# Kernel tuning notes

Hardware: AMD Instinct MI355X
Metric: run time of the kernel (lower is better)

## Reference

```python
import jax, jax.numpy as jnp
import numpy as np

ERR = 1e-6
STIFF_THR = 1e-10
EPS = 1e-12


def _normalize(x, axis=-1):
    n = jnp.linalg.norm(x, axis=axis, keepdims=True)
    return x / jnp.maximum(n, EPS)


def compute_edges(verts):
    # [B, V, 3] -> [B, V-1, 3]
    return verts[:, 1:] - verts[:, :-1]


def compute_kb(edges, restEdgeL):
    # kb[:, i] = 2 e_{i-1} x e_i / (|e_{i-1}||e_i| + e_{i-1}.e_i), kb[:, 0] = 0
    num = 2.0 * jnp.cross(edges[:, :-1], edges[:, 1:])
    den = restEdgeL[:, :-1] * restEdgeL[:, 1:] + jnp.sum(edges[:, :-1] * edges[:, 1:], axis=-1)
    kb = jnp.zeros_like(edges)
    return kb.at[:, 1:].set(num / den[..., None])


def extract_sin_cos(magnitude):
    const = 4.0
    s = jnp.sqrt(magnitude / (magnitude + const))
    c = jnp.sqrt(const / (magnitude + const))
    return s, c


def compute_m_u0(e0, init_direct):
    n0 = jnp.cross(e0, init_direct)
    return _normalize(jnp.cross(n0, e0))


def compute_bishop_frame(u0, edges, restEdgeL):
    # u0 [B,3], edges [B,E,3], restEdgeL [B,E]
    kb = compute_kb(edges, restEdgeL)                 # [B,E,3]
    mag = jnp.sum(kb * kb, axis=-1)                   # [B,E]
    sinP, cosP = extract_sin_cos(mag)
    axis = _normalize(kb)
    qw = cosP                                         # [B,E] quaternion scalar part (half angle)
    qv = sinP[..., None] * axis                       # [B,E,3] quaternion vector part
    v0 = _normalize(jnp.cross(edges[:, 0], u0))

    def step(carry, xs):
        u_p, v_p = carry
        w, xyz, e_i, c = xs                           # [B], [B,3], [B,3], [B]
        t = 2.0 * jnp.cross(xyz, u_p)
        ru = u_p + w[:, None] * t + jnp.cross(xyz, t)  # quaternion rotation of u_{i-1}
        rv = _normalize(jnp.cross(e_i, ru))
        cond = ((1.0 - c) <= ERR)[:, None]
        u_i = jnp.where(cond, u_p, ru)
        v_i = jnp.where(cond, v_p, rv)
        return (u_i, v_i), (u_i, v_i)

    xs = (jnp.swapaxes(qw[:, 1:], 0, 1), jnp.swapaxes(qv[:, 1:], 0, 1),
          jnp.swapaxes(edges[:, 1:], 0, 1), jnp.swapaxes(cosP[:, 1:], 0, 1))
    _, (us, vs) = jax.lax.scan(step, (u0, v0), xs)
    u = jnp.concatenate([u0[:, None], jnp.swapaxes(us, 0, 1)], axis=1)  # [B,E,3]
    v = jnp.concatenate([v0[:, None], jnp.swapaxes(vs, 0, 1)], axis=1)
    return u, v, kb


def compute_w(kb, m1, m2):
    # material-frame curvature: (kb.m2, -kb.m1) -> [.., 2]
    return jnp.stack([jnp.sum(kb * m2, axis=-1), -jnp.sum(kb * m1, axis=-1)], axis=-1)


def compute_material_frame(theta, m1, m2):
    cosQ = jnp.cos(theta)[..., None]
    sinQ = jnp.sin(theta)[..., None]
    m1n = cosQ * m1 + sinQ * m2
    # faithful to torch code: m2 update uses the already-updated m1
    m2n = -sinQ * m1n + cosQ * m2
    return m1n, m2n


def reference(current_vert, init_direct, restEdgeL, restRegionL, m_restWprev,
              m_restWnext, theta_full, bend_stiffness, twist_stiffness):
    edges = compute_edges(current_vert)
    u0 = compute_m_u0(edges[:, 0], init_direct)
    m1, m2, kb = compute_bishop_frame(u0, edges, restEdgeL)
    mat_m1, mat_m2 = compute_material_frame(theta_full, m1, m2)

    # Model_Energy on the (solved) theta_full
    restRegionL_unsq = restRegionL[:, 1:, None]
    oW = compute_w(kb[:, 1:], mat_m1[:, 1:], mat_m2[:, 1:])   # [B,E-1,2]
    dp = oW - m_restWprev[:, 1:]
    dn = oW - m_restWnext[:, 1:]
    bs_last = jnp.maximum(bend_stiffness[:, -1:][..., None], STIFF_THR)   # [1,1,1]
    bs_next = jnp.maximum(bend_stiffness[:, 1:][..., None], STIFF_THR)    # [1,E-1,1]
    energy = jnp.sum(0.5 * (bs_last * dp * dp + bs_next * dn * dn) / restRegionL_unsq, axis=(1, 2))
    m = theta_full[:, 1:] - theta_full[:, :-1]
    energy = energy + jnp.sum(0.5 * jnp.maximum(twist_stiffness[:, 1:], STIFF_THR) * m * m / restRegionL[:, 1:], axis=1)
    return mat_m1, mat_m2, kb, energy[:, None]


def setup_inputs() -> dict:
    key = jax.random.key(0)
    B, V = 32768, 128
    E = V - 1
    ks = jax.random.split(key, 8)
    # near-straight rod along x with small perturbations (keeps kb denominators positive)
    base = jnp.zeros((B, V, 3)).at[:, :, 0].set(jnp.arange(V, dtype=jnp.float32))
    current_vert = base + 0.05 * jax.random.normal(ks[0], (B, V, 3), dtype=jnp.float32)
    init_direct = jax.random.normal(ks[1], (B, 3), dtype=jnp.float32)
    edges = current_vert[:, 1:] - current_vert[:, :-1]
    restEdgeL = jnp.linalg.norm(edges, axis=-1)                       # [B,E]
    restRegionL = jnp.concatenate(
        [restEdgeL[:, :1], 0.5 * (restEdgeL[:, :-1] + restEdgeL[:, 1:])], axis=1)
    m_restWprev = 0.01 * jax.random.normal(ks[2], (B, E, 2), dtype=jnp.float32)
    m_restWnext = 0.01 * jax.random.normal(ks[3], (B, E, 2), dtype=jnp.float32)
    theta_full = 0.1 * jax.random.normal(ks[4], (B, E), dtype=jnp.float32)
    bend_stiffness = 5e-5 * jnp.ones((1, E), dtype=jnp.float32)
    twist_stiffness = 1e-5 * jnp.ones((1, E), dtype=jnp.float32)
    return {"current_vert": current_vert, "init_direct": init_direct,
            "restEdgeL": restEdgeL, "restRegionL": restRegionL,
            "m_restWprev": m_restWprev, "m_restWnext": m_restWnext,
            "theta_full": theta_full, "bend_stiffness": bend_stiffness,
            "twist_stiffness": twist_stiffness}
```

## Files before the change

kernel.cpp:

```cpp
#include <hip/hip_runtime.h>

#define ERRV 1e-6f
#define EPSV 1e-12f
#define THRV 1e-10f
#define MAXV 128

struct F3 { float x, y, z; };

__device__ __forceinline__ F3 mk3(float x, float y, float z){ F3 r; r.x=x; r.y=y; r.z=z; return r; }
__device__ __forceinline__ F3 cross3(F3 a, F3 b){
  return mk3(a.y*b.z - a.z*b.y, a.z*b.x - a.x*b.z, a.x*b.y - a.y*b.x);
}
__device__ __forceinline__ float dot3(F3 a, F3 b){ return a.x*b.x + a.y*b.y + a.z*b.z; }
__device__ __forceinline__ F3 norm3f(F3 a){
  float r = __builtin_amdgcn_rsqf(fmaxf(dot3(a,a), 1e-24f));
  return mk3(a.x*r, a.y*r, a.z*r);
}
__device__ __forceinline__ float4 qmul(float4 a, float4 b){
  float4 r;
  r.w = a.w*b.w - (a.x*b.x + a.y*b.y + a.z*b.z);
  r.x = a.w*b.x + b.w*a.x + (a.y*b.z - a.z*b.y);
  r.y = a.w*b.y + b.w*a.y + (a.z*b.x - a.x*b.z);
  r.z = a.w*b.z + b.w*a.z + (a.x*b.y - a.y*b.x);
  return r;
}
__device__ __forceinline__ F3 qrot(float4 q, F3 x){
  F3 v = mk3(q.x, q.y, q.z);
  F3 t = cross3(v, x);
  t = mk3(2.f*t.x, 2.f*t.y, 2.f*t.z);
  F3 ct = cross3(v, t);
  return mk3(x.x + q.w*t.x + ct.x, x.y + q.w*t.y + ct.y, x.z + q.w*t.z + ct.z);
}

extern "C" __global__ void __launch_bounds__(MAXV)
rod_energy_kernel(const float* __restrict__ verts,
                  const float* __restrict__ initd,
                  const float* __restrict__ restEdgeL,
                  const float* __restrict__ restRegionL,
                  const float* __restrict__ Wprev,
                  const float* __restrict__ Wnext,
                  const float* __restrict__ theta,
                  const float* __restrict__ bend,
                  const float* __restrict__ twist,
                  float* __restrict__ out_m1,
                  float* __restrict__ out_m2,
                  float* __restrict__ out_kb,
                  float* __restrict__ out_en,
                  int V, int E, long long bendStride, long long twistStride)
{
  __shared__ float  sV[MAXV*3];
  __shared__ float4 sQ[MAXV];
  __shared__ int    sJ[MAXV];
  __shared__ float  sW[2];

  const int b = blockIdx.x;
  const int e = threadIdx.x;
  const bool act = (e < E);

  const float* vb = verts + (size_t)b * V * 3;
  {
    const int nv4 = (V * 3) >> 2;
    if (e < nv4) ((float4*)sV)[e] = ((const float4*)vb)[e];
  }
  __syncthreads();

  #define EDGE(i) mk3(sV[((i)+1)*3+0]-sV[(i)*3+0], \
                      sV[((i)+1)*3+1]-sV[(i)*3+1], \
                      sV[((i)+1)*3+2]-sV[(i)*3+2])

  F3 edge = act ? EDGE(e) : mk3(0.f,0.f,0.f);

  const size_t rowE = (size_t)b * E;
  F3 kb = mk3(0.f, 0.f, 0.f);
  float4 q = make_float4(0.f, 0.f, 0.f, 1.f);
  int j = 0;
  if (act && e >= 1) {
    F3 ep = EDGE(e-1);
    float rl  = restEdgeL[rowE + e];
    float rlp = restEdgeL[rowE + e - 1];
    F3 cr = cross3(ep, edge);
    float den = rlp*rl + dot3(ep, edge);
    kb = mk3(2.f*cr.x/den, 2.f*cr.y/den, 2.f*cr.z/den);
    float mag  = dot3(kb, kb);
    float cosP = sqrtf(4.f/(mag+4.f));
    bool cond = (1.f - cosP) <= ERRV;
    if (!cond) {
      float r = __builtin_amdgcn_rsqf(mag + 4.f);
      q = make_float4(kb.x*r, kb.y*r, kb.z*r, 2.f*r);
      j = e;
    }
  }

  sQ[e] = q; sJ[e] = j;
  #pragma unroll
  for (int d = 1; d < MAXV; d <<= 1) {
    __syncthreads();
    float4 qp; int jp;
    const bool has = (e >= d);
    if (has) { qp = sQ[e-d]; jp = sJ[e-d]; }
    __syncthreads();
    if (has) { q = qmul(q, qp); j = (j > jp ? j : jp); sQ[e] = q; sJ[e] = j; }
  }
  __syncthreads();

  F3 e0  = EDGE(0);
  F3 dir = mk3(initd[(size_t)b*3+0], initd[(size_t)b*3+1], initd[(size_t)b*3+2]);
  F3 n0  = cross3(e0, dir);
  F3 u0  = norm3f(cross3(n0, e0));
  F3 v0  = norm3f(cross3(e0, u0));

  F3 u = u0, v = v0;
  if (act && e >= 1) {
    u = qrot(q, u0);
    if (j > 0) {
      F3 ej = EDGE(j);
      v = norm3f(cross3(ej, u));
    }
  }

  float th = act ? theta[rowE + e] : 0.f;
  float cq, sq;
  __sincosf(th, &sq, &cq);
  F3 m1 = mk3(cq*u.x + sq*v.x, cq*u.y + sq*v.y, cq*u.z + sq*v.z);
  F3 m2 = mk3(-sq*m1.x + cq*v.x, -sq*m1.y + cq*v.y, -sq*m1.z + cq*v.z);

  float contrib = 0.f;
  if (act) {
    size_t o3 = (rowE + e) * 3;
    out_m1[o3+0] = m1.x; out_m1[o3+1] = m1.y; out_m1[o3+2] = m1.z;
    out_m2[o3+0] = m2.x; out_m2[o3+1] = m2.y; out_m2[o3+2] = m2.z;
    out_kb[o3+0] = kb.x; out_kb[o3+1] = kb.y; out_kb[o3+2] = kb.z;
    if (e >= 1) {
      float rrli = __builtin_amdgcn_rcpf(restRegionL[rowE + e]);
      float wx =  dot3(kb, m2);
      float wy = -dot3(kb, m1);
      float2 wp = ((const float2*)Wprev)[rowE + e];
      float2 wn = ((const float2*)Wnext)[rowE + e];
      float dpx = wx - wp.x, dpy = wy - wp.y;
      float dnx = wx - wn.x, dny = wy - wn.y;
      float bsl = fmaxf(bend[bendStride*b + (E-1)], THRV);
      float bsn = fmaxf(bend[bendStride*b + e],     THRV);
      contrib = 0.5f*(bsl*(dpx*dpx + dpy*dpy) + bsn*(dnx*dnx + dny*dny)) * rrli;
      float dm = th - theta[rowE + e - 1];
      float ts = fmaxf(twist[twistStride*b + e], THRV);
      contrib += 0.5f*ts*dm*dm * rrli;
    }
  }

  float c = contrib;
  #pragma unroll
  for (int m = 1; m < 64; m <<= 1) c += __shfl_xor(c, m, 64);
  if ((e & 63) == 0) sW[e >> 6] = c;
  __syncthreads();
  if (e == 0) out_en[b] = sW[0] + sW[1];
  #undef EDGE
}

extern "C" void kernel_launch(void* const* d_in, const int* in_sizes, int n_in,
                              void* d_out, int out_size, void* d_ws, size_t ws_size,
                              hipStream_t stream)
{
  const float* verts       = (const float*)d_in[0];
  const float* initd       = (const float*)d_in[1];
  const float* restEdgeL   = (const float*)d_in[2];
  const float* restRegionL = (const float*)d_in[3];
  const float* Wprev       = (const float*)d_in[4];
  const float* Wnext       = (const float*)d_in[5];
  const float* theta       = (const float*)d_in[6];
  const float* bend        = (const float*)d_in[7];
  const float* twist       = (const float*)d_in[8];

  long long B = in_sizes[1] / 3;
  long long V = (long long)in_sizes[0] / (3*B);
  long long E = V - 1;
  long long bendStride  = ((long long)in_sizes[7] >= B*E) ? E : 0;
  long long twistStride = ((long long)in_sizes[8] >= B*E) ? E : 0;

  float* out_m1 = (float*)d_out;
  float* out_m2 = out_m1 + (size_t)(B*E*3);
  float* out_kb = out_m2 + (size_t)(B*E*3);
  float* out_en = out_kb + (size_t)(B*E*3);

  dim3 grid((unsigned)B), block((unsigned)V);
  hipLaunchKernelGGL(rod_energy_kernel, grid, block, 0, stream,
                     verts, initd, restEdgeL, restRegionL, Wprev, Wnext, theta,
                     bend, twist, out_m1, out_m2, out_kb, out_en,
                     (int)V, (int)E, bendStride, twistStride);
}
```

Before: 292.5 us.

## Map each rod to one wavefront with two edges per lane and shuffle scan

Each rod now runs on a single 64-lane wavefront, with every lane handling two consecutive edges, and four rods share a 256-thread block. This replaces the block-wide shared-memory quaternion scan and its many barriers. The scan becomes a local pairwise combine followed by a shuffle-based scan, and edges are gathered through shuffles. It assumes E is at most 128, and the vertex loads are unaligned float2 reads.

```diff
diff --git a/kernel.cpp b/kernel.cpp
--- a/kernel.cpp
+++ b/kernel.cpp
@@ -1,9 +1,7 @@
 #include <hip/hip_runtime.h>
 
 #define ERRV 1e-6f
-#define EPSV 1e-12f
 #define THRV 1e-10f
-#define MAXV 128
 
 struct F3 { float x, y, z; };
 
@@ -31,129 +29,168 @@
   F3 ct = cross3(v, t);
   return mk3(x.x + q.w*t.x + ct.x, x.y + q.w*t.y + ct.y, x.z + q.w*t.z + ct.z);
 }
-
-extern "C" __global__ void __launch_bounds__(MAXV)
-rod_energy_kernel(const float* __restrict__ verts,
-                  const float* __restrict__ initd,
-                  const float* __restrict__ restEdgeL,
-                  const float* __restrict__ restRegionL,
-                  const float* __restrict__ Wprev,
-                  const float* __restrict__ Wnext,
-                  const float* __restrict__ theta,
-                  const float* __restrict__ bend,
-                  const float* __restrict__ twist,
-                  float* __restrict__ out_m1,
-                  float* __restrict__ out_m2,
-                  float* __restrict__ out_kb,
-                  float* __restrict__ out_en,
-                  int V, int E, long long bendStride, long long twistStride)
+__device__ __forceinline__ float4 shflup4(float4 v, int d){
+  return make_float4(__shfl_up(v.x,d,64), __shfl_up(v.y,d,64),
+                     __shfl_up(v.z,d,64), __shfl_up(v.w,d,64));
+}
+__device__ __forceinline__ F3 shflF3(F3 v, int sl){
+  return mk3(__shfl(v.x,sl,64), __shfl(v.y,sl,64), __shfl(v.z,sl,64));
+}
+
+extern "C" __global__ void __launch_bounds__(256)
+rod_energy_wave(const float* __restrict__ verts,
+                const float* __restrict__ initd,
+                const float* __restrict__ restEdgeL,
+                const float* __restrict__ restRegionL,
+                const float* __restrict__ Wprev,
+                const float* __restrict__ Wnext,
+                const float* __restrict__ theta,
+                const float* __restrict__ bend,
+                const float* __restrict__ twist,
+                float* __restrict__ out_m1,
+                float* __restrict__ out_m2,
+                float* __restrict__ out_kb,
+                float* __restrict__ out_en,
+                int V, int E, long long B, long long bendStride, long long twistStride)
 {
-  __shared__ float  sV[MAXV*3];
-  __shared__ float4 sQ[MAXV];
-  __shared__ int    sJ[MAXV];
-  __shared__ float  sW[2];
-
-  const int b = blockIdx.x;
-  const int e = threadIdx.x;
-  const bool act = (e < E);
-
-  const float* vb = verts + (size_t)b * V * 3;
-  {
-    const int nv4 = (V * 3) >> 2;
-    if (e < nv4) ((float4*)sV)[e] = ((const float4*)vb)[e];
-  }
-  __syncthreads();
-
-  #define EDGE(i) mk3(sV[((i)+1)*3+0]-sV[(i)*3+0], \
-                      sV[((i)+1)*3+1]-sV[(i)*3+1], \
-                      sV[((i)+1)*3+2]-sV[(i)*3+2])
-
-  F3 edge = act ? EDGE(e) : mk3(0.f,0.f,0.f);
-
-  const size_t rowE = (size_t)b * E;
-  F3 kb = mk3(0.f, 0.f, 0.f);
-  float4 q = make_float4(0.f, 0.f, 0.f, 1.f);
-  int j = 0;
-  if (act && e >= 1) {
-    F3 ep = EDGE(e-1);
-    float rl  = restEdgeL[rowE + e];
-    float rlp = restEdgeL[rowE + e - 1];
-    F3 cr = cross3(ep, edge);
-    float den = rlp*rl + dot3(ep, edge);
-    kb = mk3(2.f*cr.x/den, 2.f*cr.y/den, 2.f*cr.z/den);
-    float mag  = dot3(kb, kb);
+  const int lane = threadIdx.x & 63;
+  const int wv   = threadIdx.x >> 6;
+  const long long r = (long long)blockIdx.x * 4 + wv;
+  if (r >= B) return;
+
+  const int e0i = 2*lane, e1i = 2*lane + 1;
+  const bool a0 = e0i < E, a1 = e1i < E;
+  const bool vg = (e0i + 1) < V;
+  const size_t rowE = (size_t)r * E;
+
+  const float* vb = verts + (size_t)r * V * 3;
+  float2 f01 = vg ? *(const float2*)(vb + e0i*3    ) : make_float2(0.f,0.f);
+  float2 f23 = vg ? *(const float2*)(vb + e0i*3 + 2) : make_float2(0.f,0.f);
+  float2 f45 = vg ? *(const float2*)(vb + e0i*3 + 4) : make_float2(0.f,0.f);
+  F3 vA = mk3(f01.x, f01.y, f23.x);
+  F3 vB = mk3(f23.y, f45.x, f45.y);
+  F3 vC = mk3(__shfl_down(vA.x,1,64), __shfl_down(vA.y,1,64), __shfl_down(vA.z,1,64));
+
+  F3 E0 = mk3(vB.x-vA.x, vB.y-vA.y, vB.z-vA.z);
+  F3 E1 = mk3(vC.x-vB.x, vC.y-vB.y, vC.z-vB.z);
+  F3 Ep = mk3(__shfl_up(E1.x,1,64), __shfl_up(E1.y,1,64), __shfl_up(E1.z,1,64));
+
+  float rl0 = a0 ? restEdgeL[rowE+e0i] : 0.f;
+  float rl1 = a1 ? restEdgeL[rowE+e1i] : 0.f;
+  float rlp = __shfl_up(rl1,1,64);
+
+  F3 kb0 = mk3(0.f,0.f,0.f), kb1 = mk3(0.f,0.f,0.f);
+  float4 q0 = make_float4(0.f,0.f,0.f,1.f), q1 = q0;
+  int j0 = 0, j1 = 0;
+  if (a0 && e0i >= 1) {
+    F3 cr = cross3(Ep, E0);
+    float den = rlp*rl0 + dot3(Ep, E0);
+    kb0 = mk3(2.f*cr.x/den, 2.f*cr.y/den, 2.f*cr.z/den);
+    float mag = dot3(kb0, kb0);
     float cosP = sqrtf(4.f/(mag+4.f));
-    bool cond = (1.f - cosP) <= ERRV;
-    if (!cond) {
-      float r = __builtin_amdgcn_rsqf(mag + 4.f);
-      q = make_float4(kb.x*r, kb.y*r, kb.z*r, 2.f*r);
-      j = e;
+    if (!((1.f - cosP) <= ERRV)) {
+      float rq = __builtin_amdgcn_rsqf(mag + 4.f);
+      q0 = make_float4(kb0.x*rq, kb0.y*rq, kb0.z*rq, 2.f*rq);
+      j0 = e0i;
     }
   }
-
-  sQ[e] = q; sJ[e] = j;
+  if (a1) {
+    F3 cr = cross3(E0, E1);
+    float den = rl0*rl1 + dot3(E0, E1);
+    kb1 = mk3(2.f*cr.x/den, 2.f*cr.y/den, 2.f*cr.z/den);
+    float mag = dot3(kb1, kb1);
+    float cosP = sqrtf(4.f/(mag+4.f));
+    if (!((1.f - cosP) <= ERRV)) {
+      float rq = __builtin_amdgcn_rsqf(mag + 4.f);
+      q1 = make_float4(kb1.x*rq, kb1.y*rq, kb1.z*rq, 2.f*rq);
+      j1 = e1i;
+    }
+  }
+
+  float4 S = qmul(q1, q0);
+  int J = j0 > j1 ? j0 : j1;
   #pragma unroll
-  for (int d = 1; d < MAXV; d <<= 1) {
-    __syncthreads();
-    float4 qp; int jp;
-    const bool has = (e >= d);
-    if (has) { qp = sQ[e-d]; jp = sJ[e-d]; }
-    __syncthreads();
-    if (has) { q = qmul(q, qp); j = (j > jp ? j : jp); sQ[e] = q; sJ[e] = j; }
-  }
-  __syncthreads();
-
-  F3 e0  = EDGE(0);
-  F3 dir = mk3(initd[(size_t)b*3+0], initd[(size_t)b*3+1], initd[(size_t)b*3+2]);
-  F3 n0  = cross3(e0, dir);
-  F3 u0  = norm3f(cross3(n0, e0));
-  F3 v0  = norm3f(cross3(e0, u0));
-
-  F3 u = u0, v = v0;
-  if (act && e >= 1) {
-    u = qrot(q, u0);
-    if (j > 0) {
-      F3 ej = EDGE(j);
-      v = norm3f(cross3(ej, u));
-    }
-  }
-
-  float th = act ? theta[rowE + e] : 0.f;
-  float cq, sq;
-  __sincosf(th, &sq, &cq);
-  F3 m1 = mk3(cq*u.x + sq*v.x, cq*u.y + sq*v.y, cq*u.z + sq*v.z);
-  F3 m2 = mk3(-sq*m1.x + cq*v.x, -sq*m1.y + cq*v.y, -sq*m1.z + cq*v.z);
-
+  for (int d = 1; d < 64; d <<= 1) {
+    float4 t = shflup4(S, d);
+    int tj = __shfl_up(J, d, 64);
+    if (lane >= d) { S = qmul(S, t); J = J > tj ? J : tj; }
+  }
+  float4 Sp = shflup4(S, 1);
+  int Jp = __shfl_up(J, 1, 64);
+  if (lane == 0) { Sp = make_float4(0.f,0.f,0.f,1.f); Jp = 0; }
+  const float4 M0 = qmul(q0, Sp);
+  const float4 M1 = S;
+  const int jm0 = j0 > Jp ? j0 : Jp;
+  const int jm1 = J;
+
+  F3 e0b = shflF3(E0, 0);
+  F3 dir = mk3(initd[r*3+0], initd[r*3+1], initd[r*3+2]);
+  F3 n0  = cross3(e0b, dir);
+  F3 u0g = norm3f(cross3(n0, e0b));
+  F3 v0g = norm3f(cross3(e0b, u0g));
+
+  F3 u_0 = qrot(M0, u0g);
+  F3 u_1 = qrot(M1, u0g);
+  int sl0 = jm0 >> 1, sl1 = jm1 >> 1;
+  F3 ea0 = shflF3(E0, sl0), eb0 = shflF3(E1, sl0);
+  F3 ea1 = shflF3(E0, sl1), eb1 = shflF3(E1, sl1);
+  F3 ej0 = (jm0 & 1) ? eb0 : ea0;
+  F3 ej1 = (jm1 & 1) ? eb1 : ea1;
+  F3 v_0 = (jm0 > 0) ? norm3f(cross3(ej0, u_0)) : v0g;
+  F3 v_1 = (jm1 > 0) ? norm3f(cross3(ej1, u_1)) : v0g;
+
+  float th0 = a0 ? theta[rowE+e0i] : 0.f;
+  float th1 = a1 ? theta[rowE+e1i] : 0.f;
+  float thp = __shfl_up(th1, 1, 64);
+  float s0,c0,s1,c1;
+  __sincosf(th0, &s0, &c0);
+  __sincosf(th1, &s1, &c1);
+  F3 m1_0 = mk3(c0*u_0.x + s0*v_0.x, c0*u_0.y + s0*v_0.y, c0*u_0.z + s0*v_0.z);
+  F3 m2_0 = mk3(-s0*m1_0.x + c0*v_0.x, -s0*m1_0.y + c0*v_0.y, -s0*m1_0.z + c0*v_0.z);
+  F3 m1_1 = mk3(c1*u_1.x + s1*v_1.x, c1*u_1.y + s1*v_1.y, c1*u_1.z + s1*v_1.z);
+  F3 m2_1 = mk3(-s1*m1_1.x + c1*v_1.x, -s1*m1_1.y + c1*v_1.y, -s1*m1_1.z + c1*v_1.z);
+
+  const size_t o3 = (rowE + e0i) * 3;
+  if (a0) {
+    out_m1[o3+0]=m1_0.x; out_m1[o3+1]=m1_0.y; out_m1[o3+2]=m1_0.z;
+    out_m2[o3+0]=m2_0.x; out_m2[o3+1]=m2_0.y; out_m2[o3+2]=m2_0.z;
+    out_kb[o3+0]=kb0.x;  out_kb[o3+1]=kb0.y;  out_kb[o3+2]=kb0.z;
+  }
+  if (a1) {
+    out_m1[o3+3]=m1_1.x; out_m1[o3+4]=m1_1.y; out_m1[o3+5]=m1_1.z;
+    out_m2[o3+3]=m2_1.x; out_m2[o3+4]=m2_1.y; out_m2[o3+5]=m2_1.z;
+    out_kb[o3+3]=kb1.x;  out_kb[o3+4]=kb1.y;  out_kb[o3+5]=kb1.z;
+  }
+
+  const float bsl = fmaxf(bend[bendStride*r + (E-1)], THRV);
   float contrib = 0.f;
-  if (act) {
-    size_t o3 = (rowE + e) * 3;
-    out_m1[o3+0] = m1.x; out_m1[o3+1] = m1.y; out_m1[o3+2] = m1.z;
-    out_m2[o3+0] = m2.x; out_m2[o3+1] = m2.y; out_m2[o3+2] = m2.z;
-    out_kb[o3+0] = kb.x; out_kb[o3+1] = kb.y; out_kb[o3+2] = kb.z;
-    if (e >= 1) {
-      float rrli = __builtin_amdgcn_rcpf(restRegionL[rowE + e]);
-      float wx =  dot3(kb, m2);
-      float wy = -dot3(kb, m1);
-      float2 wp = ((const float2*)Wprev)[rowE + e];
-      float2 wn = ((const float2*)Wnext)[rowE + e];
-      float dpx = wx - wp.x, dpy = wy - wp.y;
-      float dnx = wx - wn.x, dny = wy - wn.y;
-      float bsl = fmaxf(bend[bendStride*b + (E-1)], THRV);
-      float bsn = fmaxf(bend[bendStride*b + e],     THRV);
-      contrib = 0.5f*(bsl*(dpx*dpx + dpy*dpy) + bsn*(dnx*dnx + dny*dny)) * rrli;
-      float dm = th - theta[rowE + e - 1];
-      float ts = fmaxf(twist[twistStride*b + e], THRV);
-      contrib += 0.5f*ts*dm*dm * rrli;
-    }
-  }
-
-  float c = contrib;
+  if (a0 && e0i >= 1) {
+    float rrli = __builtin_amdgcn_rcpf(restRegionL[rowE+e0i]);
+    float wx =  dot3(kb0, m2_0);
+    float wy = -dot3(kb0, m1_0);
+    float2 wp = *(const float2*)(Wprev + 2*(rowE+e0i));
+    float2 wn = *(const float2*)(Wnext + 2*(rowE+e0i));
+    float dpx = wx-wp.x, dpy = wy-wp.y, dnx = wx-wn.x, dny = wy-wn.y;
+    float bsn = fmaxf(bend[bendStride*r + e0i], THRV);
+    float dm  = th0 - thp;
+    float ts  = fmaxf(twist[twistStride*r + e0i], THRV);
+    contrib += (0.5f*(bsl*(dpx*dpx+dpy*dpy) + bsn*(dnx*dnx+dny*dny)) + 0.5f*ts*dm*dm) * rrli;
+  }
+  if (a1) {
+    float rrli = __builtin_amdgcn_rcpf(restRegionL[rowE+e1i]);
+    float wx =  dot3(kb1, m2_1);
+    float wy = -dot3(kb1, m1_1);
+    float2 wp = *(const float2*)(Wprev + 2*(rowE+e1i));
+    float2 wn = *(const float2*)(Wnext + 2*(rowE+e1i));
+    float dpx = wx-wp.x, dpy = wy-wp.y, dnx = wx-wn.x, dny = wy-wn.y;
+    float bsn = fmaxf(bend[bendStride*r + e1i], THRV);
+    float dm  = th1 - th0;
+    float ts  = fmaxf(twist[twistStride*r + e1i], THRV);
+    contrib += (0.5f*(bsl*(dpx*dpx+dpy*dpy) + bsn*(dnx*dnx+dny*dny)) + 0.5f*ts*dm*dm) * rrli;
+  }
   #pragma unroll
-  for (int m = 1; m < 64; m <<= 1) c += __shfl_xor(c, m, 64);
-  if ((e & 63) == 0) sW[e >> 6] = c;
-  __syncthreads();
-  if (e == 0) out_en[b] = sW[0] + sW[1];
-  #undef EDGE
+  for (int m = 1; m < 64; m <<= 1) contrib += __shfl_xor(contrib, m, 64);
+  if (lane == 0) out_en[r] = contrib;
 }
 
 extern "C" void kernel_launch(void* const* d_in, const int* in_sizes, int n_in,
@@ -181,9 +218,9 @@
   float* out_kb = out_m2 + (size_t)(B*E*3);
   float* out_en = out_kb + (size_t)(B*E*3);
 
-  dim3 grid((unsigned)B), block((unsigned)V);
-  hipLaunchKernelGGL(rod_energy_kernel, grid, block, 0, stream,
+  dim3 grid((unsigned)((B + 3) / 4)), block(256);
+  hipLaunchKernelGGL(rod_energy_wave, grid, block, 0, stream,
                      verts, initd, restEdgeL, restRegionL, Wprev, Wnext, theta,
                      bend, twist, out_m1, out_m2, out_kb, out_en,
-                     (int)V, (int)E, bendStride, twistStride);
-}
+                     (int)V, (int)E, B, bendStride, twistStride);
+}
```

Measured after the change: 292.5 us. Within noise of the previous version (-0.0%).

## Replace shared-memory quaternion scan with wavefront shuffle scan plus cross-wave fixup

Applied to the files above, without the earlier changes.

The block-wide Hillis-Steele prefix product of quaternions previously used shared memory with two barriers per step across seven steps. It now runs an in-wavefront scan with __shfl_up over 64 lanes, then the second wave multiplies by the first wave's total, which is passed through shared memory with a single barrier. This removes most block barriers and LDS traffic. It assumes at most 128 threads (two wavefronts) and keeps the same multiplication order.

```diff
diff --git a/kernel.cpp b/kernel.cpp
--- a/kernel.cpp
+++ b/kernel.cpp
@@ -1,7 +1,6 @@
 #include <hip/hip_runtime.h>
 
 #define ERRV 1e-6f
-#define EPSV 1e-12f
 #define THRV 1e-10f
 #define MAXV 128
 
@@ -31,6 +30,10 @@
   F3 ct = cross3(v, t);
   return mk3(x.x + q.w*t.x + ct.x, x.y + q.w*t.y + ct.y, x.z + q.w*t.z + ct.z);
 }
+__device__ __forceinline__ float4 shflup4(float4 v, int d){
+  return make_float4(__shfl_up(v.x,d,64), __shfl_up(v.y,d,64),
+                     __shfl_up(v.z,d,64), __shfl_up(v.w,d,64));
+}
 
 extern "C" __global__ void __launch_bounds__(MAXV)
 rod_energy_kernel(const float* __restrict__ verts,
@@ -49,12 +52,14 @@
                   int V, int E, long long bendStride, long long twistStride)
 {
   __shared__ float  sV[MAXV*3];
-  __shared__ float4 sQ[MAXV];
-  __shared__ int    sJ[MAXV];
+  __shared__ float4 sS;
+  __shared__ int    sJt;
   __shared__ float  sW[2];
 
-  const int b = blockIdx.x;
-  const int e = threadIdx.x;
+  const int b    = blockIdx.x;
+  const int e    = threadIdx.x;
+  const int lane = e & 63;
+  const int wv   = e >> 6;
   const bool act = (e < E);
 
   const float* vb = verts + (size_t)b * V * 3;
@@ -91,17 +96,20 @@
     }
   }
 
-  sQ[e] = q; sJ[e] = j;
+  float4 S = q; int J = j;
   #pragma unroll
-  for (int d = 1; d < MAXV; d <<= 1) {
-    __syncthreads();
-    float4 qp; int jp;
-    const bool has = (e >= d);
-    if (has) { qp = sQ[e-d]; jp = sJ[e-d]; }
-    __syncthreads();
-    if (has) { q = qmul(q, qp); j = (j > jp ? j : jp); sQ[e] = q; sJ[e] = j; }
+  for (int d = 1; d < 64; d <<= 1) {
+    float4 t = shflup4(S, d);
+    int tj = __shfl_up(J, d, 64);
+    if (lane >= d) { S = qmul(S, t); J = J > tj ? J : tj; }
   }
+  if (e == 63) { sS = S; sJt = J; }
   __syncthreads();
+  if (wv == 1) {
+    S = qmul(S, sS);
+    J = J > sJt ? J : sJt;
+  }
+  q = S; j = J;
 
   F3 e0  = EDGE(0);
   F3 dir = mk3(initd[(size_t)b*3+0], initd[(size_t)b*3+1], initd[(size_t)b*3+2]);
@@ -150,7 +158,7 @@
   float c = contrib;
   #pragma unroll
   for (int m = 1; m < 64; m <<= 1) c += __shfl_xor(c, m, 64);
-  if ((e & 63) == 0) sW[e >> 6] = c;
+  if (lane == 0) sW[wv] = c;
   __syncthreads();
   if (e == 0) out_en[b] = sW[0] + sW[1];
   #undef EDGE
```

Measured after the change: 291.1 us. About the same (-0.5%).
